# Kernel tuning notes

Measured on AMD Instinct MI355X. Metric: run time of the kernel, lower is better.

## Reference

```python
import jax, jax.numpy as jnp
import numpy as np
from jax import lax

N = 2000        # nodeNum (genes)
D_IN = 256      # encodeDim
D = 256         # decodeDim
K = 10          # topkratio (k nodes kept)
C = K + 2       # cnnChannel
E_GRAPH = 64000
E_TRAIN = 50000
FLAT = C * (127 + 63 + 31)  # 2652, flattened size after conv/pool chain on length-256 signal
BN_INV = 0.9999950000375  # 1/sqrt(1+1e-5), inference BN with running stats (0,1)


def setup_inputs() -> dict:
    key = jax.random.key(0)
    ks = jax.random.split(key, 16)
    s = lambda i, shape: (jax.random.normal(ks[i], shape, jnp.float32) * 0.05)
    inp = {}
    inp["x"] = jax.random.normal(ks[0], (N, D_IN), jnp.float32)
    inp["edge_index"] = jax.random.randint(ks[1], (2, E_GRAPH), 0, N)
    inp["trainEdge"] = jax.random.randint(ks[2], (E_TRAIN, 2), 0, N)
    # SAGEConv: lin_l (neighbor aggregate, with bias) + lin_r (root, no bias)
    inp["Wl"] = s(3, (D, D_IN)); inp["bl"] = jnp.zeros((D,), jnp.float32)
    inp["Wr"] = s(4, (D, D_IN))
    inp["topk_w"] = s(5, (D,))  # TopKPooling attention vector
    inp["c1_w"] = s(6, (C, C, 2)); inp["c1_b"] = jnp.zeros((C,), jnp.float32)
    inp["c2_w"] = s(7, (C, C, 2)); inp["c2_b"] = jnp.zeros((C,), jnp.float32)
    inp["c3_w"] = s(8, (C, C, 2)); inp["c3_b"] = jnp.zeros((C,), jnp.float32)
    for nm in ("bn1", "bn2", "bn3"):
        inp[nm + "_g"] = jnp.ones((C,), jnp.float32)
        inp[nm + "_b"] = jnp.zeros((C,), jnp.float32)
    inp["bn4_g"] = jnp.ones((128,), jnp.float32); inp["bn4_b"] = jnp.zeros((128,), jnp.float32)
    inp["fc1_w"] = s(9, (128, FLAT)); inp["fc1_b"] = jnp.zeros((128,), jnp.float32)
    inp["fc2_w"] = s(10, (1, 128)); inp["fc2_b"] = jnp.zeros((1,), jnp.float32)
    return inp


def _conv1d(x, w, b):
    # x: [B, C, L], w: [O, I, 2]
    y = lax.conv_general_dilated(x, w, (1,), 'VALID', dimension_numbers=('NCH', 'OIH', 'NCH'))
    return y + b[None, :, None]


def _maxpool2(x):
    return lax.reduce_window(x, -jnp.inf, lax.max, (1, 1, 2), (1, 1, 2), 'VALID')


def _bn(x, g, b):
    # eval-mode BatchNorm1d with running_mean=0, running_var=1
    return x * (BN_INV * g)[None, :, None] + b[None, :, None]


def reference(x, edge_index, trainEdge, Wl, bl, Wr, topk_w,
              bn1_g, bn1_b, bn2_g, bn2_b, bn3_g, bn3_b, bn4_g, bn4_b,
              c1_w, c1_b, c2_w, c2_b, c3_w, c3_b, fc1_w, fc1_b, fc2_w, fc2_b):
    src, dst = edge_index[0], edge_index[1]
    # SAGEConv(mean): lin_l(mean_{j in N(i)} x_j) + lin_r(x_i), then ReLU
    agg = jnp.zeros((N, x.shape[1]), x.dtype).at[dst].add(x[src])
    deg = jnp.zeros((N,), x.dtype).at[dst].add(1.0)
    mean = agg / jnp.maximum(deg, 1.0)[:, None]
    h = jax.nn.relu(mean @ Wl.T + bl + x @ Wr.T)  # [N, D]
    # TopKPooling: score = h.w/||w||, keep top K, scale by tanh(score)
    score = h @ topk_w / jnp.linalg.norm(topk_w)
    topv, topi = lax.top_k(score, K)
    topkarr = h[topi] * jnp.tanh(topv)[:, None]  # [K, D]
    # creatDecodeInput, batched: [E, K+2, D]
    a = h[trainEdge[:, 0]][:, None, :]
    b = h[trainEdge[:, 1]][:, None, :]
    c = jnp.broadcast_to(topkarr[None], (trainEdge.shape[0], K, D))
    z = jnp.concatenate([a, b, c], axis=1)
    # calmodel CNN scorer
    z = _maxpool2(jax.nn.relu(_conv1d(_bn(z, bn1_g, bn1_b), c1_w, c1_b))); x1 = z  # [E,C,127]
    z = _maxpool2(jax.nn.relu(_conv1d(_bn(z, bn2_g, bn2_b), c2_w, c2_b))); x2 = z  # [E,C,63]
    z = _maxpool2(jax.nn.relu(_conv1d(_bn(z, bn3_g, bn3_b), c3_w, c3_b))); x3 = z  # [E,C,31]
    z = jnp.concatenate([x1, x2, x3], axis=2).reshape(x1.shape[0], -1)  # [E, FLAT]
    z = z @ fc1_w.T + fc1_b
    z = z * (BN_INV * bn4_g) + bn4_b  # bn4, eval mode
    z = z @ fc2_w.T + fc2_b
    return jax.nn.sigmoid(z).reshape(-1)  # [E]
```

## Files before the change

### kernel.cpp

```cpp
#include <hip/hip_runtime.h>
#include <hip/hip_bf16.h>
#include <math.h>

#define N_NODES 2000
#define DIN 256
#define DD 256
#define KTOP 10
#define CC 12
#define EG 64000
#define ET 50000
#define L1LEN 255
#define P1LEN 127
#define P2LEN 63
#define P3LEN 31
#define FLAT 2652
#define BN_INV 0.9999950000375f
#define CAP 96

typedef float v2 __attribute__((ext_vector_type(2)));

__device__ __forceinline__ v2 v2fma(v2 a, v2 b, v2 c) {
#if __has_builtin(__builtin_elementwise_fma)
    return __builtin_elementwise_fma(a, b, c);
#else
    v2 r; r.x = fmaf(a.x, b.x, c.x); r.y = fmaf(a.y, b.y, c.y); return r;
#endif
}
__device__ __forceinline__ v2 sp(float s) { v2 r; r.x = s; r.y = s; return r; }

#define OFF_MEAN   0
#define OFF_H      512000
#define OFF_SC     1024000
#define OFF_CNT    1026000
#define OFF_NBR    1028000
#define OFF_TAB    1220000
#define OFF_C1V    (OFF_TAB)
#define OFF_WA     (OFF_TAB + 6144)
#define OFF_WB     (OFF_TAB + 6168)
#define OFF_W2F    (OFF_TAB + 6192)
#define OFF_B2F    (OFF_TAB + 6480)
#define OFF_W3P    (OFF_TAB + 6492)
#define OFF_B3F    (OFF_TAB + 6780)
#define OFF_V2T    (OFF_TAB + 6792)
#define OFF_V3T    (OFF_TAB + 7560)
#define OFF_C0     (OFF_TAB + 7944)

__global__ void k_fill(const int* __restrict__ ei,
                       const float* __restrict__ fc1w, const float* __restrict__ fc1b,
                       const float* __restrict__ fc2w, const float* __restrict__ fc2b,
                       const float* __restrict__ bn4g, const float* __restrict__ bn4b,
                       const float* __restrict__ c1w,
                       const float* __restrict__ c2w, const float* __restrict__ c2b,
                       const float* __restrict__ c3w, const float* __restrict__ c3b,
                       const float* __restrict__ bn1g,
                       const float* __restrict__ bn2g, const float* __restrict__ bn2b,
                       const float* __restrict__ bn3g, const float* __restrict__ bn3b,
                       float* __restrict__ W) {
    const int tid = threadIdx.x, bid = blockIdx.x;
    if (bid < 250) {
        int e = bid * 256 + tid;
        int* cnt = (int*)(W + OFF_CNT);
        int* nbr = (int*)(W + OFF_NBR);
        int dst = ei[EG + e], src = ei[e];
        int slot = atomicAdd(&cnt[dst], 1);
        nbr[dst * CAP + slot] = src;
        return;
    }
    if (bid < 261) {
        int j = (bid - 250) * 256 + tid;
        if (j >= FLAT) return;
        float acc = 0.f;
        for (int k = 0; k < 128; ++k)
            acc += fc1w[k * FLAT + j] * (fc2w[k] * (BN_INV * bn4g[k]));
        int c = j / 221, pos = j - c * 221;
        if (pos < 127)      W[OFF_C1V + (c * 128 + pos) * 4 + 2] = acc;
        else if (pos < 190) W[OFF_V2T + (pos - 127) * 12 + c] = acc;
        else                W[OFF_V3T + (pos - 190) * 12 + c] = acc;
        return;
    }
    for (int t = tid; t < 288; t += 256) {
        int o = t / 24, r = t - o * 24, tt = r / 12, i = r - tt * 12;
        W[OFF_W2F + t] = c2w[o * 24 + i * 2 + tt] * (BN_INV * bn2g[i]);
        W[OFF_W3P + (tt * 12 + i) * 12 + o] = c3w[o * 24 + i * 2 + tt] * (BN_INV * bn3g[i]);
    }
    if (tid < 12) {
        float s2 = c2b[tid], s3 = c3b[tid];
        for (int i = 0; i < 12; ++i) {
            s2 += (c2w[tid * 24 + i * 2] + c2w[tid * 24 + i * 2 + 1]) * bn2b[i];
            s3 += (c3w[tid * 24 + i * 2] + c3w[tid * 24 + i * 2 + 1]) * bn3b[i];
        }
        W[OFF_B2F + tid] = s2;
        W[OFF_B3F + tid] = s3;
    }
    if (tid < 24) {
        int tt = tid / 12, o = tid - tt * 12;
        W[OFF_WA + tid] = c1w[o * 24 + tt] * (BN_INV * bn1g[0]);
        W[OFF_WB + tid] = c1w[o * 24 + 2 + tt] * (BN_INV * bn1g[1]);
    }
    if (tid == 0) {
        float c = fc2b[0];
        for (int k = 0; k < 128; ++k)
            c += fc2w[k] * (fc1b[k] * (BN_INV * bn4g[k]) + bn4b[k]);
        W[OFF_C0] = c;
    }
}

__global__ void k_gather(const float* __restrict__ x, float* __restrict__ W) {
    int w = threadIdx.x >> 6, lane = threadIdx.x & 63;
    int n = blockIdx.x * 2 + (w >> 1);
    int fo = (w & 1) * 128 + lane * 2;
    const int* cnt = (const int*)(W + OFF_CNT);
    const int* nbr = (const int*)(W + OFF_NBR);
    int dg = cnt[n];
    const int* row = nbr + n * CAP;
    float ax = 0.f, ay = 0.f;
    int j = 0;
    for (; j + 4 <= dg; j += 4) {
        int s0 = row[j], s1 = row[j + 1], s2 = row[j + 2], s3 = row[j + 3];
        float2 v0 = *(const float2*)(x + s0 * DIN + fo);
        float2 v1 = *(const float2*)(x + s1 * DIN + fo);
        float2 v2_ = *(const float2*)(x + s2 * DIN + fo);
        float2 v3 = *(const float2*)(x + s3 * DIN + fo);
        ax += v0.x + v1.x + v2_.x + v3.x;
        ay += v0.y + v1.y + v2_.y + v3.y;
    }
    for (; j < dg; ++j) {
        int s0 = row[j];
        float2 v0 = *(const float2*)(x + s0 * DIN + fo);
        ax += v0.x; ay += v0.y;
    }
    float rd = 1.0f / fmaxf((float)dg, 1.0f);
    float2 o2; o2.x = ax * rd; o2.y = ay * rd;
    *(float2*)(W + OFF_MEAN + n * DIN + fo) = o2;
}

__global__ void k_sage(const float* __restrict__ x, const float* __restrict__ Wl,
                       const float* __restrict__ bl, const float* __restrict__ Wr,
                       const float* __restrict__ tw, float* __restrict__ W) {
    __shared__ float As[32][33], Xs[32][33], Bls[32][33], Brs[32][33];
    const float* mean = W + OFF_MEAN;
    float* h = W + OFF_H;
    float* sc = W + OFF_SC;
    int tid = threadIdx.x;
    int tx = tid & 15, ty = tid >> 4;
    int n0 = blockIdx.y * 32, d0 = blockIdx.x * 32;
    int lrow = tid >> 3, lcol = (tid & 7) * 4;
    v2 acc0 = sp(0.f), acc1 = sp(0.f);
    for (int k0 = 0; k0 < DIN; k0 += 32) {
        int gn = n0 + lrow;
        float4 av, xv;
        if (gn < N_NODES) {
            av = *(const float4*)(mean + gn * DIN + k0 + lcol);
            xv = *(const float4*)(x + gn * DIN + k0 + lcol);
        } else {
            av = make_float4(0.f, 0.f, 0.f, 0.f); xv = av;
        }
        As[lrow][lcol + 0] = av.x; As[lrow][lcol + 1] = av.y;
        As[lrow][lcol + 2] = av.z; As[lrow][lcol + 3] = av.w;
        Xs[lrow][lcol + 0] = xv.x; Xs[lrow][lcol + 1] = xv.y;
        Xs[lrow][lcol + 2] = xv.z; Xs[lrow][lcol + 3] = xv.w;
        int gd = d0 + lrow;
        float4 bv = *(const float4*)(Wl + gd * DIN + k0 + lcol);
        float4 rv = *(const float4*)(Wr + gd * DIN + k0 + lcol);
        Bls[lrow][lcol + 0] = bv.x; Bls[lrow][lcol + 1] = bv.y;
        Bls[lrow][lcol + 2] = bv.z; Bls[lrow][lcol + 3] = bv.w;
        Brs[lrow][lcol + 0] = rv.x; Brs[lrow][lcol + 1] = rv.y;
        Brs[lrow][lcol + 2] = rv.z; Brs[lrow][lcol + 3] = rv.w;
        __syncthreads();
#pragma unroll
        for (int kk = 0; kk < 32; ++kk) {
            v2 b; b.x = Bls[2 * tx][kk]; b.y = Bls[2 * tx + 1][kk];
            v2 r; r.x = Brs[2 * tx][kk]; r.y = Brs[2 * tx + 1][kk];
            acc0 = v2fma(b, sp(As[2 * ty][kk]), acc0);
            acc0 = v2fma(r, sp(Xs[2 * ty][kk]), acc0);
            acc1 = v2fma(b, sp(As[2 * ty + 1][kk]), acc1);
            acc1 = v2fma(r, sp(Xs[2 * ty + 1][kk]), acc1);
        }
        __syncthreads();
    }
    float tw0 = tw[d0 + 2 * tx], tw1 = tw[d0 + 2 * tx + 1];
    float bl0 = bl[d0 + 2 * tx], bl1 = bl[d0 + 2 * tx + 1];
    float hv[2][2];
    hv[0][0] = fmaxf(acc0.x + bl0, 0.f); hv[0][1] = fmaxf(acc0.y + bl1, 0.f);
    hv[1][0] = fmaxf(acc1.x + bl0, 0.f); hv[1][1] = fmaxf(acc1.y + bl1, 0.f);
    float s0 = fmaf(hv[0][0], tw0, hv[0][1] * tw1);
    float s1 = fmaf(hv[1][0], tw0, hv[1][1] * tw1);
#pragma unroll
    for (int i = 0; i < 2; ++i) {
        int n = n0 + 2 * ty + i;
        if (n < N_NODES) {
            h[n * DD + d0 + 2 * tx] = hv[i][0];
            h[n * DD + d0 + 2 * tx + 1] = hv[i][1];
        }
    }
#pragma unroll
    for (int off = 8; off > 0; off >>= 1) {
        s0 += __shfl_xor(s0, off, 64);
        s1 += __shfl_xor(s1, off, 64);
    }
    if (tx == 0) {
        int n = n0 + 2 * ty;
        if (n < N_NODES) atomicAdd(&sc[n], s0);
        if (n + 1 < N_NODES) atomicAdd(&sc[n + 1], s1);
    }
}

__global__ void k_topk(const float* __restrict__ tw, const float* __restrict__ c1w,
                       const float* __restrict__ c1b, const float* __restrict__ bn1g,
                       const float* __restrict__ bn1b, float* __restrict__ W) {
    __shared__ float s_tt[KTOP];
    __shared__ int   s_ti[KTOP];
    int tid = threadIdx.x;
    if (tid < 64) {
        int lane = tid;
        const float* sc = W + OFF_SC;
        float v[32];
#pragma unroll
        for (int s = 0; s < 32; ++s) {
            int idx = s * 64 + lane;
            v[s] = (idx < N_NODES) ? sc[idx] : -1e30f;
        }
        float p = 0.f;
#pragma unroll
        for (int k = 0; k < 4; ++k) { float t = tw[lane + 64 * k]; p = fmaf(t, t, p); }
#pragma unroll
        for (int off = 32; off > 0; off >>= 1) p += __shfl_xor(p, off, 64);
        float rnorm = 1.0f / sqrtf(p);
#pragma unroll
        for (int k = 0; k < KTOP; ++k) {
            float m = v[0];
#pragma unroll
            for (int s = 1; s < 32; ++s) m = fmaxf(m, v[s]);
#pragma unroll
            for (int off = 32; off > 0; off >>= 1) m = fmaxf(m, __shfl_xor(m, off, 64));
            int cand = 0x7fffffff;
#pragma unroll
            for (int s = 0; s < 32; ++s)
                if (v[s] == m) cand = min(cand, s * 64 + lane);
#pragma unroll
            for (int off = 32; off > 0; off >>= 1) cand = min(cand, __shfl_xor(cand, off, 64));
#pragma unroll
            for (int s = 0; s < 32; ++s)
                if (s * 64 + lane == cand) v[s] = -1e30f;
            if (lane == 0) { s_ti[k] = cand; s_tt[k] = tanhf(m * rnorm); }
        }
    }
    __syncthreads();
    const float* h = W + OFF_H;
    const int o = blockIdx.x;
    for (int l = tid; l < L1LEN; l += 256) {
        float sum = c1b[o];
        sum += (c1w[o * 24 + 0] + c1w[o * 24 + 1]) * bn1b[0];
        sum += (c1w[o * 24 + 2] + c1w[o * 24 + 3]) * bn1b[1];
#pragma unroll
        for (int r = 0; r < KTOP; ++r) {
            int ch = r + 2;
            float tv = s_tt[r];
            float sr = BN_INV * bn1g[ch];
            float br = bn1b[ch];
            const float* hr = h + s_ti[r] * DD;
            float v0 = fmaf(hr[l], tv * sr, br);
            float v1 = fmaf(hr[l + 1], tv * sr, br);
            sum += c1w[o * 24 + ch * 2] * v0 + c1w[o * 24 + ch * 2 + 1] * v1;
        }
        W[OFF_C1V + (o * 128 + (l >> 1)) * 4 + (l & 1)] = sum;
    }
}

__launch_bounds__(128, 6)
__global__ void k_edges(const float* __restrict__ h, const int* __restrict__ te,
                        const float* __restrict__ W, float* __restrict__ out) {
    __shared__ float s1[2][CC][128];
    const int tid = threadIdx.x;
    const int w = tid >> 6, lane = tid & 63;
    const int e = blockIdx.x * 2 + w;

    int na = __builtin_amdgcn_readfirstlane(te[2 * e]);
    int nb = __builtin_amdgcn_readfirstlane(te[2 * e + 1]);
    const float* ha = h + na * DD;
    const float* hb = h + nb * DD;
    const float4* c1v = (const float4*)(W + OFF_C1V);
    const float* wa = W + OFF_WA;
    const float* wb = W + OFF_WB;
    const float* w2 = W + OFF_W2F;
    const float* b2 = W + OFF_B2F;
    const float* w3p = W + OFF_W3P;
    const float* b3 = W + OFF_B3F;
    const float4* v2t = (const float4*)(W + OFF_V2T);
    const float4* v3t = (const float4*)(W + OFF_V3T);

    float dot0 = 0.f, dot1 = 0.f;

#pragma unroll
    for (int rep = 0; rep < 2; ++rep) {
        int p = lane + rep * 64;
        if (p < P1LEN) {
            float2 a01 = *(const float2*)(ha + 2 * p);
            float  a2  = ha[2 * p + 2];
            float2 b01 = *(const float2*)(hb + 2 * p);
            float  b2v = hb[2 * p + 2];
            v2 va0; va0.x = a01.x; va0.y = a01.y;
            v2 va1; va1.x = a01.y; va1.y = a2;
            v2 vb0; vb0.x = b01.x; vb0.y = b01.y;
            v2 vb1; vb1.x = b01.y; vb1.y = b2v;
#pragma unroll
            for (int o = 0; o < CC; ++o) {
                float4 cv = c1v[o * 128 + p];
                v2 u; u.x = cv.x; u.y = cv.y;
                u = v2fma(sp(wa[o]), va0, u);
                u = v2fma(sp(wa[12 + o]), va1, u);
                u = v2fma(sp(wb[o]), vb0, u);
                u = v2fma(sp(wb[12 + o]), vb1, u);
                float r = fmaxf(fmaxf(u.x, u.y), 0.0f);
                s1[w][o][p] = r;
                if (o & 1) dot1 = fmaf(r, cv.z, dot1);
                else       dot0 = fmaf(r, cv.z, dot0);
            }
        }
    }
    __builtin_amdgcn_wave_barrier();

    float r2[CC];
#pragma unroll
    for (int i = 0; i < CC; ++i) r2[i] = 0.f;
    if (lane < P2LEN) {
        int p = lane;
        v2 evo[CC], ovE[CC];
#pragma unroll
        for (int i = 0; i < CC; ++i) {
            float2 t2 = *(const float2*)(&s1[w][i][2 * p]);
            float e1 = s1[w][i][2 * p + 2];
            evo[i].x = t2.x; evo[i].y = t2.y;
            ovE[i].x = t2.y; ovE[i].y = e1;
        }
        const float4* vrow = v2t + p * 3;
#pragma unroll
        for (int g = 0; g < 3; ++g) {
            float4 q = vrow[g];
#pragma unroll
            for (int oo = 0; oo < 4; ++oo) {
                const int o = g * 4 + oo;
                v2 a = sp(b2[o]);
#pragma unroll
                for (int i = 0; i < CC; ++i) {
                    a = v2fma(sp(w2[o * 24 + i]), evo[i], a);
                    a = v2fma(sp(w2[o * 24 + 12 + i]), ovE[i], a);
                }
                float r = fmaxf(fmaxf(a.x, a.y), 0.0f);
                r2[o] = r;
                float vv = (oo == 0) ? q.x : (oo == 1) ? q.y : (oo == 2) ? q.z : q.w;
                if (o & 1) dot1 = fmaf(r, vv, dot1);
                else       dot0 = fmaf(r, vv, dot0);
            }
        }
    }

    {
        float vq1[CC];
#pragma unroll
        for (int i = 0; i < CC; ++i) vq1[i] = __shfl_down(r2[i], 1, 64);
        bool take = ((lane & 1) == 0) && (lane < 62);
        int t = lane >> 1;
        float4 ug0 = v3t[t * 3 + 0], ug1 = v3t[t * 3 + 1], ug2 = v3t[t * 3 + 2];
#pragma unroll
        for (int op = 0; op < 6; ++op) {
            const int o = 2 * op;
            v2 a; a.x = b3[o]; a.y = b3[o + 1];
#pragma unroll
            for (int i = 0; i < CC; ++i) {
                a = v2fma(sp(r2[i]), *(const v2*)(w3p + i * 12 + o), a);
                a = v2fma(sp(vq1[i]), *(const v2*)(w3p + (12 + i) * 12 + o), a);
            }
            float pnx = __shfl_xor(a.x, 1, 64);
            float pny = __shfl_xor(a.y, 1, 64);
            float r0 = fmaxf(fmaxf(a.x, pnx), 0.0f);
            float r1 = fmaxf(fmaxf(a.y, pny), 0.0f);
            if (take) {
                const float4 ug = (op < 2) ? ug0 : (op < 4) ? ug1 : ug2;
                float w0 = (op & 1) ? ug.z : ug.x;
                float w1 = (op & 1) ? ug.w : ug.y;
                dot0 = fmaf(r0, w0, dot0);
                dot1 = fmaf(r1, w1, dot1);
            }
        }
    }

    float dot = dot0 + dot1;
#pragma unroll
    for (int off = 32; off > 0; off >>= 1) dot += __shfl_xor(dot, off, 64);
    if (lane == 0) {
        float tt = dot + W[OFF_C0];
        out[e] = 1.0f / (1.0f + expf(-tt));
    }
}

extern "C" void kernel_launch(void* const* d_in, const int* in_sizes, int n_in,
                              void* d_out, int out_size, void* d_ws, size_t ws_size,
                              hipStream_t stream) {
    const float* x    = (const float*)d_in[0];
    const int*   ei   = (const int*)d_in[1];
    const int*   te   = (const int*)d_in[2];
    const float* Wl   = (const float*)d_in[3];
    const float* bl   = (const float*)d_in[4];
    const float* Wr   = (const float*)d_in[5];
    const float* tw   = (const float*)d_in[6];
    const float* c1w  = (const float*)d_in[7];
    const float* c1b  = (const float*)d_in[8];
    const float* c2w  = (const float*)d_in[9];
    const float* c2b  = (const float*)d_in[10];
    const float* c3w  = (const float*)d_in[11];
    const float* c3b  = (const float*)d_in[12];
    const float* bn1g = (const float*)d_in[13];
    const float* bn1b = (const float*)d_in[14];
    const float* bn2g = (const float*)d_in[15];
    const float* bn2b = (const float*)d_in[16];
    const float* bn3g = (const float*)d_in[17];
    const float* bn3b = (const float*)d_in[18];
    const float* bn4g = (const float*)d_in[19];
    const float* bn4b = (const float*)d_in[20];
    const float* fc1w = (const float*)d_in[21];
    const float* fc1b = (const float*)d_in[22];
    const float* fc2w = (const float*)d_in[23];
    const float* fc2b = (const float*)d_in[24];
    float* W   = (float*)d_ws;
    float* out = (float*)d_out;

    hipMemsetAsync(W + OFF_SC, 0, 4000 * sizeof(float), stream);
    k_fill<<<262, 256, 0, stream>>>(ei, fc1w, fc1b, fc2w, fc2b, bn4g, bn4b, c1w,
                                    c2w, c2b, c3w, c3b, bn1g, bn2g, bn2b, bn3g, bn3b, W);
    k_gather<<<1000, 256, 0, stream>>>(x, W);
    dim3 g2(8, 63);
    k_sage<<<g2, 256, 0, stream>>>(x, Wl, bl, Wr, tw, W);
    k_topk<<<12, 256, 0, stream>>>(tw, c1w, c1b, bn1g, bn1b, W);
    k_edges<<<ET / 2, 128, 0, stream>>>(W + OFF_H, te, W, out);
}
```

Measured before the change: 161.7 us.

## Split SAGE root GEMM into fill kernel and keep conv1 outputs in registers

The x@Wr.T root half of the SAGE layer moves into k_fill as extra blocks, so it runs alongside the edge-count setup, and k_sage now only does the mean@Wl part and adds the stored partial. In k_edges each lane now computes four conv1 positions from one float4 load and passes neighbour values with cross-lane shuffles instead of through shared memory. The conv1 constant table is re-laid out to match, and blocks grow to four edges. The aim is to remove the LDS round-trip and barrier in the per-edge kernel and to shorten the SAGE critical path. In exchange register pressure rises and the launch bounds change.

Result: faster. 151.6 us (median of 2 runs) (-6.3%).

```diff
diff --git a/kernel.cpp b/kernel.cpp
--- a/kernel.cpp
+++ b/kernel.cpp
@@ -34,18 +34,20 @@
 #define OFF_CNT    1026000
 #define OFF_NBR    1028000
 #define OFF_TAB    1220000
-#define OFF_C1V    (OFF_TAB)
-#define OFF_WA     (OFF_TAB + 6144)
-#define OFF_WB     (OFF_TAB + 6168)
-#define OFF_W2F    (OFF_TAB + 6192)
-#define OFF_B2F    (OFF_TAB + 6480)
-#define OFF_W3P    (OFF_TAB + 6492)
-#define OFF_B3F    (OFF_TAB + 6780)
-#define OFF_V2T    (OFF_TAB + 6792)
-#define OFF_V3T    (OFF_TAB + 7560)
-#define OFF_C0     (OFF_TAB + 7944)
-
-__global__ void k_fill(const int* __restrict__ ei,
+#define OFF_C1Q    (OFF_TAB)
+#define OFF_V1P    (OFF_TAB + 3072)
+#define OFF_WA     (OFF_TAB + 4608)
+#define OFF_WB     (OFF_TAB + 4632)
+#define OFF_W2F    (OFF_TAB + 4656)
+#define OFF_B2F    (OFF_TAB + 4944)
+#define OFF_W3P    (OFF_TAB + 4956)
+#define OFF_B3F    (OFF_TAB + 5244)
+#define OFF_V2T    (OFF_TAB + 5256)
+#define OFF_V3T    (OFF_TAB + 6024)
+#define OFF_C0     (OFF_TAB + 6408)
+
+__global__ void k_fill(const int* __restrict__ ei, const float* __restrict__ x,
+                       const float* __restrict__ Wr,
                        const float* __restrict__ fc1w, const float* __restrict__ fc1b,
                        const float* __restrict__ fc2w, const float* __restrict__ fc2b,
                        const float* __restrict__ bn4g, const float* __restrict__ bn4b,
@@ -56,6 +58,7 @@
                        const float* __restrict__ bn2g, const float* __restrict__ bn2b,
                        const float* __restrict__ bn3g, const float* __restrict__ bn3b,
                        float* __restrict__ W) {
+    __shared__ float Xs[32][33], Brs[32][33];
     const int tid = threadIdx.x, bid = blockIdx.x;
     if (bid < 250) {
         int e = bid * 256 + tid;
@@ -73,35 +76,75 @@
         for (int k = 0; k < 128; ++k)
             acc += fc1w[k * FLAT + j] * (fc2w[k] * (BN_INV * bn4g[k]));
         int c = j / 221, pos = j - c * 221;
-        if (pos < 127)      W[OFF_C1V + (c * 128 + pos) * 4 + 2] = acc;
+        if (pos < 127)      W[OFF_V1P + c * 128 + pos] = acc;
         else if (pos < 190) W[OFF_V2T + (pos - 127) * 12 + c] = acc;
         else                W[OFF_V3T + (pos - 190) * 12 + c] = acc;
         return;
     }
-    for (int t = tid; t < 288; t += 256) {
-        int o = t / 24, r = t - o * 24, tt = r / 12, i = r - tt * 12;
-        W[OFF_W2F + t] = c2w[o * 24 + i * 2 + tt] * (BN_INV * bn2g[i]);
-        W[OFF_W3P + (tt * 12 + i) * 12 + o] = c3w[o * 24 + i * 2 + tt] * (BN_INV * bn3g[i]);
-    }
-    if (tid < 12) {
-        float s2 = c2b[tid], s3 = c3b[tid];
-        for (int i = 0; i < 12; ++i) {
-            s2 += (c2w[tid * 24 + i * 2] + c2w[tid * 24 + i * 2 + 1]) * bn2b[i];
-            s3 += (c3w[tid * 24 + i * 2] + c3w[tid * 24 + i * 2 + 1]) * bn3b[i];
-        }
-        W[OFF_B2F + tid] = s2;
-        W[OFF_B3F + tid] = s3;
-    }
-    if (tid < 24) {
-        int tt = tid / 12, o = tid - tt * 12;
-        W[OFF_WA + tid] = c1w[o * 24 + tt] * (BN_INV * bn1g[0]);
-        W[OFF_WB + tid] = c1w[o * 24 + 2 + tt] * (BN_INV * bn1g[1]);
-    }
-    if (tid == 0) {
-        float c = fc2b[0];
-        for (int k = 0; k < 128; ++k)
-            c += fc2w[k] * (fc1b[k] * (BN_INV * bn4g[k]) + bn4b[k]);
-        W[OFF_C0] = c;
+    if (bid == 261) {
+        for (int t = tid; t < 288; t += 256) {
+            int o = t / 24, r = t - o * 24, tt = r / 12, i = r - tt * 12;
+            W[OFF_W2F + t] = c2w[o * 24 + i * 2 + tt] * (BN_INV * bn2g[i]);
+            W[OFF_W3P + (tt * 12 + i) * 12 + o] = c3w[o * 24 + i * 2 + tt] * (BN_INV * bn3g[i]);
+        }
+        if (tid < 12) {
+            float s2 = c2b[tid], s3 = c3b[tid];
+            for (int i = 0; i < 12; ++i) {
+                s2 += (c2w[tid * 24 + i * 2] + c2w[tid * 24 + i * 2 + 1]) * bn2b[i];
+                s3 += (c3w[tid * 24 + i * 2] + c3w[tid * 24 + i * 2 + 1]) * bn3b[i];
+            }
+            W[OFF_B2F + tid] = s2;
+            W[OFF_B3F + tid] = s3;
+            W[OFF_V1P + tid * 128 + 127] = 0.f;
+        }
+        if (tid < 24) {
+            int tt = tid / 12, o = tid - tt * 12;
+            W[OFF_WA + tid] = c1w[o * 24 + tt] * (BN_INV * bn1g[0]);
+            W[OFF_WB + tid] = c1w[o * 24 + 2 + tt] * (BN_INV * bn1g[1]);
+        }
+        if (tid == 0) {
+            float c = fc2b[0];
+            for (int k = 0; k < 128; ++k)
+                c += fc2w[k] * (fc1b[k] * (BN_INV * bn4g[k]) + bn4b[k]);
+            W[OFF_C0] = c;
+        }
+        return;
+    }
+    {
+        int id = bid - 262;
+        int bx = id & 7, by = id >> 3;
+        int n0 = by * 32, d0 = bx * 32;
+        int tx = tid & 15, ty = tid >> 4;
+        int lrow = tid >> 3, lcol = (tid & 7) * 4;
+        v2 acc0 = sp(0.f), acc1 = sp(0.f);
+        for (int k0 = 0; k0 < DIN; k0 += 32) {
+            int gn = n0 + lrow;
+            float4 xv = (gn < N_NODES) ? *(const float4*)(x + gn * DIN + k0 + lcol)
+                                       : make_float4(0.f, 0.f, 0.f, 0.f);
+            Xs[lrow][lcol + 0] = xv.x; Xs[lrow][lcol + 1] = xv.y;
+            Xs[lrow][lcol + 2] = xv.z; Xs[lrow][lcol + 3] = xv.w;
+            float4 rv = *(const float4*)(Wr + (d0 + lrow) * DIN + k0 + lcol);
+            Brs[lrow][lcol + 0] = rv.x; Brs[lrow][lcol + 1] = rv.y;
+            Brs[lrow][lcol + 2] = rv.z; Brs[lrow][lcol + 3] = rv.w;
+            __syncthreads();
+#pragma unroll
+            for (int kk = 0; kk < 32; ++kk) {
+                v2 r; r.x = Brs[2 * tx][kk]; r.y = Brs[2 * tx + 1][kk];
+                acc0 = v2fma(r, sp(Xs[2 * ty][kk]), acc0);
+                acc1 = v2fma(r, sp(Xs[2 * ty + 1][kk]), acc1);
+            }
+            __syncthreads();
+        }
+        float* h = W + OFF_H;
+#pragma unroll
+        for (int i = 0; i < 2; ++i) {
+            int n = n0 + 2 * ty + i;
+            if (n < N_NODES) {
+                v2 a = (i == 0) ? acc0 : acc1;
+                h[n * DD + d0 + 2 * tx] = a.x;
+                h[n * DD + d0 + 2 * tx + 1] = a.y;
+            }
+        }
     }
 }
 
@@ -134,10 +177,9 @@
     *(float2*)(W + OFF_MEAN + n * DIN + fo) = o2;
 }
 
-__global__ void k_sage(const float* __restrict__ x, const float* __restrict__ Wl,
-                       const float* __restrict__ bl, const float* __restrict__ Wr,
+__global__ void k_sage(const float* __restrict__ Wl, const float* __restrict__ bl,
                        const float* __restrict__ tw, float* __restrict__ W) {
-    __shared__ float As[32][33], Xs[32][33], Bls[32][33], Brs[32][33];
+    __shared__ float As[32][33], Bls[32][33];
     const float* mean = W + OFF_MEAN;
     float* h = W + OFF_H;
     float* sc = W + OFF_SC;
@@ -148,49 +190,36 @@
     v2 acc0 = sp(0.f), acc1 = sp(0.f);
     for (int k0 = 0; k0 < DIN; k0 += 32) {
         int gn = n0 + lrow;
-        float4 av, xv;
-        if (gn < N_NODES) {
-            av = *(const float4*)(mean + gn * DIN + k0 + lcol);
-            xv = *(const float4*)(x + gn * DIN + k0 + lcol);
-        } else {
-            av = make_float4(0.f, 0.f, 0.f, 0.f); xv = av;
-        }
+        float4 av = (gn < N_NODES) ? *(const float4*)(mean + gn * DIN + k0 + lcol)
+                                   : make_float4(0.f, 0.f, 0.f, 0.f);
         As[lrow][lcol + 0] = av.x; As[lrow][lcol + 1] = av.y;
         As[lrow][lcol + 2] = av.z; As[lrow][lcol + 3] = av.w;
-        Xs[lrow][lcol + 0] = xv.x; Xs[lrow][lcol + 1] = xv.y;
-        Xs[lrow][lcol + 2] = xv.z; Xs[lrow][lcol + 3] = xv.w;
-        int gd = d0 + lrow;
-        float4 bv = *(const float4*)(Wl + gd * DIN + k0 + lcol);
-        float4 rv = *(const float4*)(Wr + gd * DIN + k0 + lcol);
+        float4 bv = *(const float4*)(Wl + (d0 + lrow) * DIN + k0 + lcol);
         Bls[lrow][lcol + 0] = bv.x; Bls[lrow][lcol + 1] = bv.y;
         Bls[lrow][lcol + 2] = bv.z; Bls[lrow][lcol + 3] = bv.w;
-        Brs[lrow][lcol + 0] = rv.x; Brs[lrow][lcol + 1] = rv.y;
-        Brs[lrow][lcol + 2] = rv.z; Brs[lrow][lcol + 3] = rv.w;
         __syncthreads();
 #pragma unroll
         for (int kk = 0; kk < 32; ++kk) {
             v2 b; b.x = Bls[2 * tx][kk]; b.y = Bls[2 * tx + 1][kk];
-            v2 r; r.x = Brs[2 * tx][kk]; r.y = Brs[2 * tx + 1][kk];
             acc0 = v2fma(b, sp(As[2 * ty][kk]), acc0);
-            acc0 = v2fma(r, sp(Xs[2 * ty][kk]), acc0);
             acc1 = v2fma(b, sp(As[2 * ty + 1][kk]), acc1);
-            acc1 = v2fma(r, sp(Xs[2 * ty + 1][kk]), acc1);
         }
         __syncthreads();
     }
     float tw0 = tw[d0 + 2 * tx], tw1 = tw[d0 + 2 * tx + 1];
     float bl0 = bl[d0 + 2 * tx], bl1 = bl[d0 + 2 * tx + 1];
-    float hv[2][2];
-    hv[0][0] = fmaxf(acc0.x + bl0, 0.f); hv[0][1] = fmaxf(acc0.y + bl1, 0.f);
-    hv[1][0] = fmaxf(acc1.x + bl0, 0.f); hv[1][1] = fmaxf(acc1.y + bl1, 0.f);
-    float s0 = fmaf(hv[0][0], tw0, hv[0][1] * tw1);
-    float s1 = fmaf(hv[1][0], tw0, hv[1][1] * tw1);
+    float s0 = 0.f, s1 = 0.f;
 #pragma unroll
     for (int i = 0; i < 2; ++i) {
         int n = n0 + 2 * ty + i;
         if (n < N_NODES) {
-            h[n * DD + d0 + 2 * tx] = hv[i][0];
-            h[n * DD + d0 + 2 * tx + 1] = hv[i][1];
+            v2 a = (i == 0) ? acc0 : acc1;
+            float h0 = fmaxf(a.x + bl0 + h[n * DD + d0 + 2 * tx], 0.f);
+            float h1 = fmaxf(a.y + bl1 + h[n * DD + d0 + 2 * tx + 1], 0.f);
+            h[n * DD + d0 + 2 * tx] = h0;
+            h[n * DD + d0 + 2 * tx + 1] = h1;
+            float s = fmaf(h0, tw0, h1 * tw1);
+            if (i == 0) s0 = s; else s1 = s;
         }
     }
 #pragma unroll
@@ -248,38 +277,41 @@
     __syncthreads();
     const float* h = W + OFF_H;
     const int o = blockIdx.x;
-    for (int l = tid; l < L1LEN; l += 256) {
-        float sum = c1b[o];
-        sum += (c1w[o * 24 + 0] + c1w[o * 24 + 1]) * bn1b[0];
-        sum += (c1w[o * 24 + 2] + c1w[o * 24 + 3]) * bn1b[1];
-#pragma unroll
-        for (int r = 0; r < KTOP; ++r) {
-            int ch = r + 2;
-            float tv = s_tt[r];
-            float sr = BN_INV * bn1g[ch];
-            float br = bn1b[ch];
-            const float* hr = h + s_ti[r] * DD;
-            float v0 = fmaf(hr[l], tv * sr, br);
-            float v1 = fmaf(hr[l + 1], tv * sr, br);
-            sum += c1w[o * 24 + ch * 2] * v0 + c1w[o * 24 + ch * 2 + 1] * v1;
-        }
-        W[OFF_C1V + (o * 128 + (l >> 1)) * 4 + (l & 1)] = sum;
-    }
-}
-
-__launch_bounds__(128, 6)
+    for (int l = tid; l < 256; l += 256) {
+        float sum = 0.f;
+        if (l < L1LEN) {
+            sum = c1b[o];
+            sum += (c1w[o * 24 + 0] + c1w[o * 24 + 1]) * bn1b[0];
+            sum += (c1w[o * 24 + 2] + c1w[o * 24 + 3]) * bn1b[1];
+#pragma unroll
+            for (int r = 0; r < KTOP; ++r) {
+                int ch = r + 2;
+                float tv = s_tt[r];
+                float sr = BN_INV * bn1g[ch];
+                float br = bn1b[ch];
+                const float* hr = h + s_ti[r] * DD;
+                float v0 = fmaf(hr[l], tv * sr, br);
+                float v1 = fmaf(hr[l + 1], tv * sr, br);
+                sum += c1w[o * 24 + ch * 2] * v0 + c1w[o * 24 + ch * 2 + 1] * v1;
+            }
+        }
+        W[OFF_C1Q + o * 256 + l] = sum;
+    }
+}
+
+__launch_bounds__(256, 7)
 __global__ void k_edges(const float* __restrict__ h, const int* __restrict__ te,
                         const float* __restrict__ W, float* __restrict__ out) {
-    __shared__ float s1[2][CC][128];
     const int tid = threadIdx.x;
     const int w = tid >> 6, lane = tid & 63;
-    const int e = blockIdx.x * 2 + w;
+    const int e = blockIdx.x * 4 + w;
 
     int na = __builtin_amdgcn_readfirstlane(te[2 * e]);
     int nb = __builtin_amdgcn_readfirstlane(te[2 * e + 1]);
     const float* ha = h + na * DD;
     const float* hb = h + nb * DD;
-    const float4* c1v = (const float4*)(W + OFF_C1V);
+    const float4* c1q = (const float4*)(W + OFF_C1Q);
+    const float2* v1p = (const float2*)(W + OFF_V1P);
     const float* wa = W + OFF_WA;
     const float* wb = W + OFF_WB;
     const float* w2 = W + OFF_W2F;
@@ -291,66 +323,65 @@
 
     float dot0 = 0.f, dot1 = 0.f;
 
-#pragma unroll
-    for (int rep = 0; rep < 2; ++rep) {
-        int p = lane + rep * 64;
-        if (p < P1LEN) {
-            float2 a01 = *(const float2*)(ha + 2 * p);
-            float  a2  = ha[2 * p + 2];
-            float2 b01 = *(const float2*)(hb + 2 * p);
-            float  b2v = hb[2 * p + 2];
-            v2 va0; va0.x = a01.x; va0.y = a01.y;
-            v2 va1; va1.x = a01.y; va1.y = a2;
-            v2 vb0; vb0.x = b01.x; vb0.y = b01.y;
-            v2 vb1; vb1.x = b01.y; vb1.y = b2v;
-#pragma unroll
-            for (int o = 0; o < CC; ++o) {
-                float4 cv = c1v[o * 128 + p];
-                v2 u; u.x = cv.x; u.y = cv.y;
-                u = v2fma(sp(wa[o]), va0, u);
-                u = v2fma(sp(wa[12 + o]), va1, u);
-                u = v2fma(sp(wb[o]), vb0, u);
-                u = v2fma(sp(wb[12 + o]), vb1, u);
-                float r = fmaxf(fmaxf(u.x, u.y), 0.0f);
-                s1[w][o][p] = r;
-                if (o & 1) dot1 = fmaf(r, cv.z, dot1);
-                else       dot0 = fmaf(r, cv.z, dot0);
-            }
-        }
-    }
-    __builtin_amdgcn_wave_barrier();
+    float rA[CC], rB[CC];
+    {
+        float4 a4 = *(const float4*)(ha + 4 * lane);
+        float4 b4 = *(const float4*)(hb + 4 * lane);
+        float ha4 = __shfl_down(a4.x, 1, 64);
+        float hb4 = __shfl_down(b4.x, 1, 64);
+        v2 a01, a12, a23, a34, b01, b12, b23, b34;
+        a01.x = a4.x; a01.y = a4.y;  a12.x = a4.y; a12.y = a4.z;
+        a23.x = a4.z; a23.y = a4.w;  a34.x = a4.w; a34.y = ha4;
+        b01.x = b4.x; b01.y = b4.y;  b12.x = b4.y; b12.y = b4.z;
+        b23.x = b4.z; b23.y = b4.w;  b34.x = b4.w; b34.y = hb4;
+#pragma unroll
+        for (int o = 0; o < CC; ++o) {
+            float4 c = c1q[o * 64 + lane];
+            float2 vp = v1p[o * 64 + lane];
+            float wa0 = wa[o], wa1 = wa[12 + o], wb0 = wb[o], wb1 = wb[12 + o];
+            v2 u01; u01.x = c.x; u01.y = c.y;
+            v2 u23; u23.x = c.z; u23.y = c.w;
+            u01 = v2fma(sp(wa0), a01, u01); u01 = v2fma(sp(wa1), a12, u01);
+            u01 = v2fma(sp(wb0), b01, u01); u01 = v2fma(sp(wb1), b12, u01);
+            u23 = v2fma(sp(wa0), a23, u23); u23 = v2fma(sp(wa1), a34, u23);
+            u23 = v2fma(sp(wb0), b23, u23); u23 = v2fma(sp(wb1), b34, u23);
+            float ra = fmaxf(fmaxf(u01.x, u01.y), 0.0f);
+            float rb = fmaxf(fmaxf(u23.x, u23.y), 0.0f);
+            rA[o] = ra; rB[o] = rb;
+            dot0 = fmaf(ra, vp.x, dot0);
+            dot1 = fmaf(rb, vp.y, dot1);
+        }
+    }
 
     float r2[CC];
 #pragma unroll
     for (int i = 0; i < CC; ++i) r2[i] = 0.f;
-    if (lane < P2LEN) {
-        int p = lane;
-        v2 evo[CC], ovE[CC];
-#pragma unroll
-        for (int i = 0; i < CC; ++i) {
-            float2 t2 = *(const float2*)(&s1[w][i][2 * p]);
-            float e1 = s1[w][i][2 * p + 2];
-            evo[i].x = t2.x; evo[i].y = t2.y;
-            ovE[i].x = t2.y; ovE[i].y = e1;
-        }
-        const float4* vrow = v2t + p * 3;
-#pragma unroll
-        for (int g = 0; g < 3; ++g) {
-            float4 q = vrow[g];
-#pragma unroll
-            for (int oo = 0; oo < 4; ++oo) {
-                const int o = g * 4 + oo;
-                v2 a = sp(b2[o]);
-#pragma unroll
-                for (int i = 0; i < CC; ++i) {
-                    a = v2fma(sp(w2[o * 24 + i]), evo[i], a);
-                    a = v2fma(sp(w2[o * 24 + 12 + i]), ovE[i], a);
+    {
+        float ve1[CC];
+#pragma unroll
+        for (int i = 0; i < CC; ++i) ve1[i] = __shfl_down(rA[i], 1, 64);
+        if (lane < P2LEN) {
+            const float4* vrow = v2t + lane * 3;
+#pragma unroll
+            for (int g = 0; g < 3; ++g) {
+                float4 q = vrow[g];
+#pragma unroll
+                for (int oo = 0; oo < 4; ++oo) {
+                    const int o = g * 4 + oo;
+                    v2 a = sp(b2[o]);
+#pragma unroll
+                    for (int i = 0; i < CC; ++i) {
+                        v2 evo; evo.x = rA[i]; evo.y = rB[i];
+                        v2 ovE; ovE.x = rB[i]; ovE.y = ve1[i];
+                        a = v2fma(sp(w2[o * 24 + i]), evo, a);
+                        a = v2fma(sp(w2[o * 24 + 12 + i]), ovE, a);
+                    }
+                    float r = fmaxf(fmaxf(a.x, a.y), 0.0f);
+                    r2[o] = r;
+                    float vv = (oo == 0) ? q.x : (oo == 1) ? q.y : (oo == 2) ? q.z : q.w;
+                    if (o & 1) dot1 = fmaf(r, vv, dot1);
+                    else       dot0 = fmaf(r, vv, dot0);
                 }
-                float r = fmaxf(fmaxf(a.x, a.y), 0.0f);
-                r2[o] = r;
-                float vv = (oo == 0) ? q.x : (oo == 1) ? q.y : (oo == 2) ? q.z : q.w;
-                if (o & 1) dot1 = fmaf(r, vv, dot1);
-                else       dot0 = fmaf(r, vv, dot0);
             }
         }
     }
@@ -426,11 +457,11 @@
     float* out = (float*)d_out;
 
     hipMemsetAsync(W + OFF_SC, 0, 4000 * sizeof(float), stream);
-    k_fill<<<262, 256, 0, stream>>>(ei, fc1w, fc1b, fc2w, fc2b, bn4g, bn4b, c1w,
+    k_fill<<<766, 256, 0, stream>>>(ei, x, Wr, fc1w, fc1b, fc2w, fc2b, bn4g, bn4b, c1w,
                                     c2w, c2b, c3w, c3b, bn1g, bn2g, bn2b, bn3g, bn3b, W);
     k_gather<<<1000, 256, 0, stream>>>(x, W);
     dim3 g2(8, 63);
-    k_sage<<<g2, 256, 0, stream>>>(x, Wl, bl, Wr, tw, W);
+    k_sage<<<g2, 256, 0, stream>>>(Wl, bl, tw, W);
     k_topk<<<12, 256, 0, stream>>>(tw, c1w, c1b, bn1g, bn1b, W);
-    k_edges<<<ET / 2, 128, 0, stream>>>(W + OFF_H, te, W, out);
-}
+    k_edges<<<ET / 4, 256, 0, stream>>>(W + OFF_H, te, W, out);
+}
```
